# Performance work log

Hardware: AMD Instinct MI355X
Metric: run time of the kernel (lower is better)

## Reference

```python
import jax, jax.numpy as jnp
import numpy as np
import math

NUM_HEADS = 12


def _rope_tables(nph, npw, half_head_dim):
    # grid coords: x = column index, y = row index, flattened row-major
    rows = jnp.arange(nph, dtype=jnp.float32)
    cols = jnp.arange(npw, dtype=jnp.float32)
    gy, gx = jnp.meshgrid(rows, cols, indexing='ij')
    coords = jnp.stack([gx.ravel(), gy.ravel()], axis=1)  # [N, 2]
    cmin = coords.min(axis=0, keepdims=True)
    cmax = coords.max(axis=0, keepdims=True)
    nc = (coords - cmin) / (cmax - cmin + 1e-8)
    div = jnp.exp(jnp.arange(0, half_head_dim, 2, dtype=jnp.float32)
                  * (-(math.log(10000.0) / half_head_dim)))  # [half/2]
    px = nc[:, 0:1] * div  # [N, half/2]
    py = nc[:, 1:2] * div
    rep = lambda t: jnp.repeat(t, 2, axis=-1)  # interleave: even/odd slots get same value
    return rep(jnp.cos(px)), rep(jnp.sin(px)), rep(jnp.cos(py)), rep(jnp.sin(py))


def _apply_rope(t, cos_x, sin_x, cos_y, sin_y):
    # t: [B, H, N, Dh]; tables: [N, Dh//2] broadcast over B, H
    half = t.shape[-1] // 2
    tx, ty = t[..., :half], t[..., half:]
    rx = tx * cos_x + jnp.roll(tx, 1, axis=-1) * sin_x
    ry = ty * cos_y + jnp.roll(ty, 1, axis=-1) * sin_y
    return jnp.concatenate([rx, ry], axis=-1)


def setup_inputs() -> dict:
    key = jax.random.key(0)
    k1, k2, k3 = jax.random.split(key, 3)
    B, S, E = 32, 577, 768  # 24*24 patches + 1 CLS token
    x = jax.random.normal(k1, (B, S, E), dtype=jnp.float32)
    w_qkv = jax.random.normal(k2, (3 * E, E), dtype=jnp.float32) * 0.02
    w_proj = jax.random.normal(k3, (E, E), dtype=jnp.float32) * 0.02
    return {"x": x, "w_qkv": w_qkv, "w_proj": w_proj,
            "num_patches_h": 24, "num_patches_w": 24}


def reference(x, w_qkv, w_proj, num_patches_h, num_patches_w):
    B, S, E = x.shape
    H = NUM_HEADS
    Dh = E // H
    # QKV projection (bias=False)
    qkv = jnp.einsum('bse,fe->bsf', x, w_qkv).reshape(B, S, 3, H, Dh)
    qkv = jnp.transpose(qkv, (2, 0, 3, 1, 4))  # [3, B, H, S, Dh]
    q, k, v = qkv[0], qkv[1], qkv[2]
    # 2D RoPE on patch tokens only (CLS at position 0 unchanged)
    cx, sx, cy, sy = _rope_tables(num_patches_h, num_patches_w, Dh // 2)
    q_patch = _apply_rope(q[:, :, 1:], cx, sx, cy, sy)
    k_patch = _apply_rope(k[:, :, 1:], cx, sx, cy, sy)
    q = jnp.concatenate([q[:, :, :1], q_patch], axis=2)
    k = jnp.concatenate([k[:, :, :1], k_patch], axis=2)
    # scaled dot-product attention (standard backend, dropout=0)
    attn = jnp.einsum('bhqd,bhkd->bhqk', q, k) * (Dh ** -0.5)
    attn = jax.nn.softmax(attn, axis=-1)
    out = jnp.einsum('bhqk,bhkd->bhqd', attn, v)
    out = jnp.transpose(out, (0, 2, 1, 3)).reshape(B, S, E)
    return out @ w_proj.T
```

## Files before the change

### kernel.cpp

```cpp
#include <hip/hip_runtime.h>
#include <hip/hip_bf16.h>
#include <cstdint>


typedef __attribute__((ext_vector_type(8))) short bf16x8;
typedef __attribute__((ext_vector_type(4))) float f32x4;

#define MFMA16(a, b, c) __builtin_amdgcn_mfma_f32_16x16x32_bf16((a), (b), (c), 0, 0, 0)

#define S_LEN 577
#define NHEAD 12
#define DHEAD 64
#define EMB   768
#define F3    2304
#define NT_KV 10
#define BUFO  (128 * 32)

__device__ __forceinline__ void gload_lds16(const __hip_bfloat16* g, __hip_bfloat16* l) {
    __builtin_amdgcn_global_load_lds(
        (const __attribute__((address_space(1))) unsigned int*)g,
        (__attribute__((address_space(3))) unsigned int*)l, 16, 0, 0);
}

__device__ __forceinline__ uint4 cvt8_f32(float4 a, float4 b) {
    union { uint4 u; __hip_bfloat16 h[8]; } r;
    r.h[0] = __float2bfloat16(a.x); r.h[1] = __float2bfloat16(a.y);
    r.h[2] = __float2bfloat16(a.z); r.h[3] = __float2bfloat16(a.w);
    r.h[4] = __float2bfloat16(b.x); r.h[5] = __float2bfloat16(b.y);
    r.h[6] = __float2bfloat16(b.z); r.h[7] = __float2bfloat16(b.w);
    return r.u;
}

template<bool AF32, bool BF32, bool CF32>
__global__ __launch_bounds__(256) void gemm_a_dma(
    const void* __restrict__ Av, int lda,
    const void* __restrict__ Bv, int ldb,
    void* __restrict__ Cv, int M, int N, int K)
{
    __shared__ __hip_bfloat16 As[2 * BUFO];
    __shared__ __hip_bfloat16 Bs[2 * BUFO];

    const int t      = threadIdx.x;
    const int l      = t & 63;
    const int w      = t >> 6;
    const int lane15 = l & 15;
    const int quad   = l >> 4;

    const int n0 = blockIdx.x * 128;
    const int m0 = blockIdx.y * 128;
    const int wm = (w >> 1) * 64;
    const int wn = (w & 1) * 64;

    const int srow   = t >> 2;
    const int schunk = t & 3;
    const int fsw    = (t >> 3) & 3;
    const int gchunk = schunk ^ fsw;

    int ar0 = m0 + srow;       if (ar0 > M - 1) ar0 = M - 1;
    int ar1 = m0 + 64 + srow;  if (ar1 > M - 1) ar1 = M - 1;
    const int br0 = n0 + srow;
    const int br1 = n0 + 64 + srow;

    const size_t a0off = (size_t)ar0 * lda + gchunk * 8;
    const size_t a1off = (size_t)ar1 * lda + gchunk * 8;
    const size_t b0off = (size_t)br0 * ldb + gchunk * 8;
    const size_t b1off = (size_t)br1 * ldb + gchunk * 8;

    __hip_bfloat16* lAs0 = As + srow * 32 + schunk * 8;
    __hip_bfloat16* lAs1 = As + (64 + srow) * 32 + schunk * 8;
    __hip_bfloat16* lBs0 = Bs + srow * 32 + schunk * 8;
    __hip_bfloat16* lBs1 = Bs + (64 + srow) * 32 + schunk * 8;

    const int rsw = (quad ^ ((lane15 >> 1) & 3)) * 8;

    f32x4 acc[4][4] = {};

    if constexpr (AF32) {
        const float* qa0 = (const float*)Av + a0off;
        const float* qa1 = (const float*)Av + a1off;
        *(uint4*)lAs0 = cvt8_f32(*(const float4*)qa0, *(const float4*)(qa0 + 4));
        *(uint4*)lAs1 = cvt8_f32(*(const float4*)qa1, *(const float4*)(qa1 + 4));
    } else {
        gload_lds16((const __hip_bfloat16*)Av + a0off, lAs0);
        gload_lds16((const __hip_bfloat16*)Av + a1off, lAs1);
    }
    if constexpr (BF32) {
        const float* pb0 = (const float*)Bv + b0off;
        const float* pb1 = (const float*)Bv + b1off;
        *(uint4*)lBs0 = cvt8_f32(*(const float4*)pb0, *(const float4*)(pb0 + 4));
        *(uint4*)lBs1 = cvt8_f32(*(const float4*)pb1, *(const float4*)(pb1 + 4));
    } else {
        gload_lds16((const __hip_bfloat16*)Bv + b0off, lBs0);
        gload_lds16((const __hip_bfloat16*)Bv + b1off, lBs1);
    }
    __syncthreads();

#define GEMM_STEP(kn, CO, NO)                                                 \
    {                                                                         \
        const bool has_next = (kn) < K;                                       \
        float4 a0 = {}, a1 = {}, a2 = {}, a3 = {};                            \
        float4 g0 = {}, g1 = {}, g2 = {}, g3 = {};                            \
        if (has_next) {                                                       \
            if constexpr (AF32) {                                             \
                const float* qa0 = (const float*)Av + a0off + (kn);           \
                const float* qa1 = (const float*)Av + a1off + (kn);           \
                a0 = *(const float4*)qa0; a1 = *(const float4*)(qa0 + 4);     \
                a2 = *(const float4*)qa1; a3 = *(const float4*)(qa1 + 4);     \
            } else {                                                          \
                gload_lds16((const __hip_bfloat16*)Av + a0off + (kn), lAs0 + (NO)); \
                gload_lds16((const __hip_bfloat16*)Av + a1off + (kn), lAs1 + (NO)); \
            }                                                                 \
            if constexpr (BF32) {                                             \
                const float* pb0 = (const float*)Bv + b0off + (kn);           \
                const float* pb1 = (const float*)Bv + b1off + (kn);           \
                g0 = *(const float4*)pb0; g1 = *(const float4*)(pb0 + 4);     \
                g2 = *(const float4*)pb1; g3 = *(const float4*)(pb1 + 4);     \
            } else {                                                          \
                gload_lds16((const __hip_bfloat16*)Bv + b0off + (kn), lBs0 + (NO)); \
                gload_lds16((const __hip_bfloat16*)Bv + b1off + (kn), lBs1 + (NO)); \
            }                                                                 \
        }                                                                     \
        bf16x8 a[4], b[4];                                                    \
        _Pragma("unroll")                                                     \
        for (int i = 0; i < 4; ++i)                                           \
            a[i] = *(const bf16x8*)(As + (CO) + (wm + i * 16 + lane15) * 32 + rsw); \
        _Pragma("unroll")                                                     \
        for (int j = 0; j < 4; ++j)                                           \
            b[j] = *(const bf16x8*)(Bs + (CO) + (wn + j * 16 + lane15) * 32 + rsw); \
        _Pragma("unroll")                                                     \
        for (int i = 0; i < 4; ++i)                                           \
            _Pragma("unroll")                                                 \
            for (int j = 0; j < 4; ++j)                                       \
                acc[i][j] = MFMA16(a[i], b[j], acc[i][j]);                    \
        if (has_next) {                                                       \
            if constexpr (AF32) {                                             \
                *(uint4*)(lAs0 + (NO)) = cvt8_f32(a0, a1);                    \
                *(uint4*)(lAs1 + (NO)) = cvt8_f32(a2, a3);                    \
            }                                                                 \
            if constexpr (BF32) {                                             \
                *(uint4*)(lBs0 + (NO)) = cvt8_f32(g0, g1);                    \
                *(uint4*)(lBs1 + (NO)) = cvt8_f32(g2, g3);                    \
            }                                                                 \
        }                                                                     \
        __syncthreads();                                                      \
    }

    for (int k0 = 0; k0 < K; k0 += 64) {
        GEMM_STEP(k0 + 32, 0,    BUFO)
        GEMM_STEP(k0 + 64, BUFO, 0)
    }
#undef GEMM_STEP

    #pragma unroll
    for (int i = 0; i < 4; ++i) {
        #pragma unroll
        for (int r = 0; r < 4; ++r) {
            const int m = m0 + wm + i * 16 + quad * 4 + r;
            if (m < M) {
                #pragma unroll
                for (int j = 0; j < 4; ++j) {
                    const int n = n0 + wn + j * 16 + lane15;
                    if constexpr (CF32)
                        ((float*)Cv)[(size_t)m * N + n] = acc[i][j][r];
                    else
                        ((__hip_bfloat16*)Cv)[(size_t)m * N + n] = __float2bfloat16(acc[i][j][r]);
                }
            }
        }
    }
}

__global__ __launch_bounds__(256) void rope_kernel(__hip_bfloat16* __restrict__ qkv)
{
    const int p = blockIdx.x;
    const int b = blockIdx.y;
    const int l = threadIdx.x & 63;
    const int w = threadIdx.x >> 6;

    const int jj   = l & 31;
    const float i2 = (float)((jj >> 1) * 2);
    const float dv = __expf(-i2 * 0.28782313662425576f);
    const float inv = 1.0f / (23.0f + 1e-8f);
    const float cx = (float)(p % 24) * inv;
    const float cy = (float)(p / 24) * inv;
    const float ang = ((l < 32) ? cx : cy) * dv;
    const float c = __cosf(ang);
    const float s = __sinf(ang);
    const int nb = (l & 32) | ((jj + 31) & 31);

    const size_t rowbase = ((size_t)(b * S_LEN + 1 + p)) * F3;

    for (int pr = w; pr < 24; pr += 4) {
        const int part = pr / 12;
        const int h    = pr % 12;
        const size_t off = rowbase + (size_t)part * EMB + h * DHEAD + l;
        float v  = __bfloat162float(qkv[off]);
        float vp = __shfl(v, nb, 64);
        qkv[off] = __float2bfloat16(v * c + vp * s);
    }
}

__global__ __launch_bounds__(512) void attn_kernel(
    const __hip_bfloat16* __restrict__ qkv,
    __hip_bfloat16* __restrict__ attn_out, int ldo)
{
    __shared__ __hip_bfloat16 Qs[128][72];
    __shared__ __hip_bfloat16 Ks[64][72];
    __shared__ __hip_bfloat16 Vt[64][72];

    const int t      = threadIdx.x;
    const int l      = t & 63;
    const int w      = t >> 6;
    const int lane15 = l & 15;
    const int quad   = l >> 4;

    const int q0 = blockIdx.x * 128;
    const int h  = blockIdx.y;
    const int b  = blockIdx.z;

    const int krow = t >> 3, kseg = t & 7;
    const int vs   = t & 63, vdg = t >> 6;

    uint4 ku, vu;
    {
        int gk = krow; if (gk > S_LEN - 1) gk = S_LEN - 1;
        ku = ((const uint4*)(qkv + (size_t)(b * S_LEN + gk) * F3 + EMB + h * DHEAD))[kseg];
        int gv = vs;  if (gv > S_LEN - 1) gv = S_LEN - 1;
        vu = ((const uint4*)(qkv + (size_t)(b * S_LEN + gv) * F3 + 2 * EMB + h * DHEAD))[vdg];
    }

    {
        const int row = t >> 2, seg = t & 3;
        int gq = q0 + row; if (gq > S_LEN - 1) gq = S_LEN - 1;
        const uint4* src = (const uint4*)(qkv + (size_t)(b * S_LEN + gq) * F3 + h * DHEAD + seg * 16);
        uint4 u0 = src[0], u1 = src[1];
        const __hip_bfloat16* e0 = (const __hip_bfloat16*)&u0;
        const __hip_bfloat16* e1 = (const __hip_bfloat16*)&u1;
        #pragma unroll
        for (int i = 0; i < 8; ++i) {
            Qs[row][seg * 16 + i]     = __float2bfloat16(__bfloat162float(e0[i]) * 0.125f);
            Qs[row][seg * 16 + 8 + i] = __float2bfloat16(__bfloat162float(e1[i]) * 0.125f);
        }
    }
    __syncthreads();

    bf16x8 qf0 = *(const bf16x8*)&Qs[w * 16 + lane15][quad * 8];
    bf16x8 qf1 = *(const bf16x8*)&Qs[w * 16 + lane15][32 + quad * 8];

    f32x4 o[4] = {};
    float m_i = -3.0e38f;
    float l_i = 0.f;

    for (int ti = 0; ti < NT_KV; ++ti) {
        __syncthreads();
        *(uint4*)&Ks[krow][kseg * 8] = ku;
        {
            const __hip_bfloat16* e0 = (const __hip_bfloat16*)&vu;
            #pragma unroll
            for (int i = 0; i < 8; ++i)
                Vt[vdg * 8 + i][vs] = e0[i];
        }
        if (ti + 1 < NT_KV) {
            int gk = (ti + 1) * 64 + krow; if (gk > S_LEN - 1) gk = S_LEN - 1;
            ku = ((const uint4*)(qkv + (size_t)(b * S_LEN + gk) * F3 + EMB + h * DHEAD))[kseg];
            int gv = (ti + 1) * 64 + vs;  if (gv > S_LEN - 1) gv = S_LEN - 1;
            vu = ((const uint4*)(qkv + (size_t)(b * S_LEN + gv) * F3 + 2 * EMB + h * DHEAD))[vdg];
        }
        asm volatile("s_waitcnt lgkmcnt(0)" ::: "memory");
        __builtin_amdgcn_s_barrier();
        asm volatile("" ::: "memory");

        f32x4 sf[4];
        #pragma unroll
        for (int nt = 0; nt < 4; ++nt) {
            f32x4 z = {0.f, 0.f, 0.f, 0.f};
            bf16x8 k0f = *(const bf16x8*)&Ks[nt * 16 + lane15][quad * 8];
            bf16x8 k1f = *(const bf16x8*)&Ks[nt * 16 + lane15][32 + quad * 8];
            z = MFMA16(k0f, qf0, z);
            z = MFMA16(k1f, qf1, z);
            sf[nt] = z;
        }
        const int s0 = ti * 64;
        #pragma unroll
        for (int nt = 0; nt < 4; ++nt)
            #pragma unroll
            for (int r = 0; r < 4; ++r)
                if (s0 + nt * 16 + quad * 4 + r >= S_LEN) sf[nt][r] = -1e30f;

        float mx = fmaxf(fmaxf(sf[0][0], sf[0][1]), fmaxf(sf[0][2], sf[0][3]));
        #pragma unroll
        for (int nt = 1; nt < 4; ++nt)
            mx = fmaxf(mx, fmaxf(fmaxf(sf[nt][0], sf[nt][1]), fmaxf(sf[nt][2], sf[nt][3])));
        mx = fmaxf(mx, __shfl_xor(mx, 16, 64));
        mx = fmaxf(mx, __shfl_xor(mx, 32, 64));

        const float mnew  = fmaxf(m_i, mx);
        const float alpha = __expf(m_i - mnew);
        m_i = mnew;

        float sum = 0.f;
        #pragma unroll
        for (int nt = 0; nt < 4; ++nt) {
            #pragma unroll
            for (int r = 0; r < 4; ++r) {
                sf[nt][r] = __expf(sf[nt][r] - mnew);
                sum += sf[nt][r];
            }
        }
        sum += __shfl_xor(sum, 16, 64);
        sum += __shfl_xor(sum, 32, 64);
        l_i = l_i * alpha + sum;

        float af[4];
        #pragma unroll
        for (int r = 0; r < 4; ++r)
            af[r] = __shfl(alpha, quad * 4 + r, 64);
        #pragma unroll
        for (int ci = 0; ci < 4; ++ci)
            #pragma unroll
            for (int r = 0; r < 4; ++r)
                o[ci][r] *= af[r];

        #pragma unroll
        for (int nt = 0; nt < 4; ++nt)
            #pragma unroll
            for (int r = 0; r < 4; ++r)
                Qs[w * 16 + lane15][nt * 16 + quad * 4 + r] = __float2bfloat16(sf[nt][r]);
        asm volatile("s_waitcnt lgkmcnt(0)" ::: "memory");

        #pragma unroll
        for (int s32 = 0; s32 < 2; ++s32) {
            bf16x8 pa = *(const bf16x8*)&Qs[w * 16 + lane15][s32 * 32 + quad * 8];
            #pragma unroll
            for (int ci = 0; ci < 4; ++ci) {
                bf16x8 vb = *(const bf16x8*)&Vt[ci * 16 + lane15][s32 * 32 + quad * 8];
                o[ci] = MFMA16(pa, vb, o[ci]);
            }
        }
    }

    #pragma unroll
    for (int r = 0; r < 4; ++r) {
        const float lr = __shfl(l_i, quad * 4 + r, 64);
        const int q = q0 + w * 16 + quad * 4 + r;
        if (q < S_LEN) {
            const float rl = 1.0f / lr;
            #pragma unroll
            for (int ci = 0; ci < 4; ++ci) {
                attn_out[(size_t)(b * S_LEN + q) * ldo + h * DHEAD + ci * 16 + lane15] =
                    __float2bfloat16(o[ci][r] * rl);
            }
        }
    }
}

extern "C" void kernel_launch(void* const* d_in, const int* in_sizes, int n_in,
                              void* d_out, int out_size, void* d_ws, size_t ws_size,
                              hipStream_t stream) {
    const float* x      = (const float*)d_in[0];
    const float* w_qkv  = (const float*)d_in[1];
    const float* w_proj = (const float*)d_in[2];
    for (int i = 0; i < n_in; ++i) {
        if      (in_sizes[i] == 32 * S_LEN * EMB) x      = (const float*)d_in[i];
        else if (in_sizes[i] == F3 * EMB)         w_qkv  = (const float*)d_in[i];
        else if (in_sizes[i] == EMB * EMB)        w_proj = (const float*)d_in[i];
    }
    float* out = (float*)d_out;

    const int Mrows = 32 * S_LEN;

    __hip_bfloat16* qkv = (__hip_bfloat16*)d_ws;

    gemm_a_dma<true, true, false><<<dim3(F3 / 128, (Mrows + 127) / 128), 256, 0, stream>>>(
        x, EMB, w_qkv, EMB, qkv, Mrows, F3, EMB);
    rope_kernel<<<dim3(576, 32), 256, 0, stream>>>(qkv);
    attn_kernel<<<dim3((S_LEN + 127) / 128, NHEAD, 32), 512, 0, stream>>>(qkv, qkv, F3);
    gemm_a_dma<false, true, true><<<dim3(EMB / 128, (Mrows + 127) / 128), 256, 0, stream>>>(
        qkv, F3, w_proj, EMB, out, Mrows, EMB, EMB);
}
```

Baseline: 433.8 us.

## Pre-convert QKV GEMM inputs to bf16, lazy softmax rescale, MFMA priority

Adds a separate kernel that converts x and w_qkv from fp32 to bf16 into the output buffer before the QKV GEMM, so the GEMM can use its bf16 DMA-to-LDS path for both operands instead of converting fp32 on the fly. In attention, the online-softmax rescale of the running max, sum and accumulator is skipped unless some lane's max grows by more than 8, which cuts exp and multiply work per tile at the cost of letting unnormalised values reach up to e^8 before rescaling. It also raises wave priority around the MFMA blocks. The conversion adds an extra pass over x and the weights through global memory.

New measurement: 388.0 us. 1.12x faster.

```diff
diff --git a/kernel.cpp b/kernel.cpp
--- a/kernel.cpp
+++ b/kernel.cpp
@@ -29,6 +29,18 @@
     r.h[4] = __float2bfloat16(b.x); r.h[5] = __float2bfloat16(b.y);
     r.h[6] = __float2bfloat16(b.z); r.h[7] = __float2bfloat16(b.w);
     return r.u;
+}
+
+__device__ __forceinline__ uint4 load8_f32(const float* p) {
+    return cvt8_f32(*(const float4*)p, *(const float4*)(p + 4));
+}
+
+__global__ __launch_bounds__(256) void cvt_f32_bf16(
+    const float* __restrict__ src, __hip_bfloat16* __restrict__ dst, int n8)
+{
+    const int i = blockIdx.x * 256 + threadIdx.x;
+    if (i < n8)
+        *(uint4*)(dst + (size_t)i * 8) = load8_f32(src + (size_t)i * 8);
 }
 
 template<bool AF32, bool BF32, bool CF32>
@@ -271,6 +283,7 @@
         asm volatile("" ::: "memory");
 
         f32x4 sf[4];
+        __builtin_amdgcn_s_setprio(1);
         #pragma unroll
         for (int nt = 0; nt < 4; ++nt) {
             f32x4 z = {0.f, 0.f, 0.f, 0.f};
@@ -280,6 +293,7 @@
             z = MFMA16(k1f, qf1, z);
             sf[nt] = z;
         }
+        __builtin_amdgcn_s_setprio(0);
         const int s0 = ti * 64;
         #pragma unroll
         for (int nt = 0; nt < 4; ++nt)
@@ -294,32 +308,34 @@
         mx = fmaxf(mx, __shfl_xor(mx, 16, 64));
         mx = fmaxf(mx, __shfl_xor(mx, 32, 64));
 
-        const float mnew  = fmaxf(m_i, mx);
-        const float alpha = __expf(m_i - mnew);
-        m_i = mnew;
+        if (!__all(mx - m_i <= 8.0f)) {
+            const float mnew  = fmaxf(m_i, mx);
+            const float alpha = __expf(m_i - mnew);
+            m_i = mnew;
+            l_i *= alpha;
+            float af[4];
+            #pragma unroll
+            for (int r = 0; r < 4; ++r)
+                af[r] = __shfl(alpha, quad * 4 + r, 64);
+            #pragma unroll
+            for (int ci = 0; ci < 4; ++ci)
+                #pragma unroll
+                for (int r = 0; r < 4; ++r)
+                    o[ci][r] *= af[r];
+        }
 
         float sum = 0.f;
         #pragma unroll
         for (int nt = 0; nt < 4; ++nt) {
             #pragma unroll
             for (int r = 0; r < 4; ++r) {
-                sf[nt][r] = __expf(sf[nt][r] - mnew);
+                sf[nt][r] = __expf(sf[nt][r] - m_i);
                 sum += sf[nt][r];
             }
         }
         sum += __shfl_xor(sum, 16, 64);
         sum += __shfl_xor(sum, 32, 64);
-        l_i = l_i * alpha + sum;
-
-        float af[4];
-        #pragma unroll
-        for (int r = 0; r < 4; ++r)
-            af[r] = __shfl(alpha, quad * 4 + r, 64);
-        #pragma unroll
-        for (int ci = 0; ci < 4; ++ci)
-            #pragma unroll
-            for (int r = 0; r < 4; ++r)
-                o[ci][r] *= af[r];
+        l_i += sum;
 
         #pragma unroll
         for (int nt = 0; nt < 4; ++nt)
@@ -328,6 +344,7 @@
                 Qs[w * 16 + lane15][nt * 16 + quad * 4 + r] = __float2bfloat16(sf[nt][r]);
         asm volatile("s_waitcnt lgkmcnt(0)" ::: "memory");
 
+        __builtin_amdgcn_s_setprio(1);
         #pragma unroll
         for (int s32 = 0; s32 < 2; ++s32) {
             bf16x8 pa = *(const bf16x8*)&Qs[w * 16 + lane15][s32 * 32 + quad * 8];
@@ -337,6 +354,7 @@
                 o[ci] = MFMA16(pa, vb, o[ci]);
             }
         }
+        __builtin_amdgcn_s_setprio(0);
     }
 
     #pragma unroll
@@ -368,11 +386,17 @@
     float* out = (float*)d_out;
 
     const int Mrows = 32 * S_LEN;
+    const int NX    = Mrows * EMB;
+    const int NWQ   = F3 * EMB;
 
     __hip_bfloat16* qkv = (__hip_bfloat16*)d_ws;
-
-    gemm_a_dma<true, true, false><<<dim3(F3 / 128, (Mrows + 127) / 128), 256, 0, stream>>>(
-        x, EMB, w_qkv, EMB, qkv, Mrows, F3, EMB);
+    __hip_bfloat16* xb  = (__hip_bfloat16*)d_out;
+    __hip_bfloat16* wb  = xb + (size_t)NX;
+
+    cvt_f32_bf16<<<NX / 8 / 256, 256, 0, stream>>>(x, xb, NX / 8);
+    cvt_f32_bf16<<<NWQ / 8 / 256, 256, 0, stream>>>(w_qkv, wb, NWQ / 8);
+    gemm_a_dma<false, false, false><<<dim3(F3 / 128, (Mrows + 127) / 128), 256, 0, stream>>>(
+        xb, EMB, wb, EMB, qkv, Mrows, F3, EMB);
     rope_kernel<<<dim3(576, 32), 256, 0, stream>>>(qkv);
     attn_kernel<<<dim3((S_LEN + 127) / 128, NHEAD, 32), 512, 0, stream>>>(qkv, qkv, F3);
     gemm_a_dma<false, true, true><<<dim3(EMB / 128, (Mrows + 127) / 128), 256, 0, stream>>>(
```
